# Performance work log

Hardware: AMD Instinct MI355X
Metric: run time of the kernel (lower is better)

The kernel has to match this reference:

```python
import jax, jax.numpy as jnp
import numpy as np

N, E, D, H, C, G = 80000, 1280000, 64, 64, 5, 512


def setup_inputs() -> dict:
    key = jax.random.key(0)
    ks = jax.random.split(key, 8)
    h = jax.random.normal(ks[0], (N, D), jnp.float32)
    src = jax.random.randint(ks[1], (E,), 0, N)
    dst = jax.random.randint(ks[2], (E,), 0, N)
    graph_ids = jnp.sort(jax.random.randint(ks[3], (N,), 0, G))
    # Glorot-ish init for weights
    W1 = jax.random.normal(ks[4], (D, H), jnp.float32) * (1.0 / np.sqrt(D))
    b1 = jnp.zeros((H,), jnp.float32)
    W2 = jax.random.normal(ks[5], (H, H), jnp.float32) * (1.0 / np.sqrt(H))
    b2 = jnp.zeros((H,), jnp.float32)
    Wc = jax.random.normal(ks[6], (H, C), jnp.float32) * (1.0 / np.sqrt(H))
    bc = jnp.zeros((C,), jnp.float32)
    return dict(h=h, src=src, dst=dst, graph_ids=graph_ids,
                W1=W1, b1=b1, W2=W2, b2=b2, Wc=Wc, bc=bc, num_graphs=G)


def reference(h, src, dst, graph_ids, W1, b1, W2, b2, Wc, bc, num_graphs):
    n = h.shape[0]
    ones_e = jnp.ones(src.shape[0], h.dtype)
    # DGL GraphConv norm='both': symmetric normalization, degrees clamped to >=1
    out_deg = jnp.clip(jax.ops.segment_sum(ones_e, src, num_segments=n), 1.0)
    in_deg = jnp.clip(jax.ops.segment_sum(ones_e, dst, num_segments=n), 1.0)
    norm_src = jax.lax.rsqrt(out_deg)  # [N]
    norm_dst = jax.lax.rsqrt(in_deg)   # [N]

    def graph_conv(x, W, b):
        x = x * norm_src[:, None]                                   # scale by D_out^{-1/2}
        agg = jax.ops.segment_sum(x[src], dst, num_segments=n)      # sparse A^T x (copy_u + sum)
        agg = agg * norm_dst[:, None]                               # scale by D_in^{-1/2}
        return agg @ W + b

    h1 = jax.nn.relu(graph_conv(h, W1, b1))
    h2 = jax.nn.relu(graph_conv(h1, W2, b2))

    # dgl.mean_nodes: per-graph mean pooling over nodes
    cnt = jnp.clip(jax.ops.segment_sum(jnp.ones(n, h.dtype), graph_ids,
                                       num_segments=num_graphs), 1.0)
    hg = jax.ops.segment_sum(h2, graph_ids, num_segments=num_graphs) / cnt[:, None]
    return hg @ Wc + bc  # [G, C] logits
```

## Files before the change

### kernel.cpp

```cpp
#include <hip/hip_runtime.h>
#include <hip/hip_bf16.h>


#define NBK 160

typedef __attribute__((ext_vector_type(8))) short bf16x8;
typedef __attribute__((ext_vector_type(4))) float f32x4;

__device__ __forceinline__ float bflo(unsigned u) { return __uint_as_float(u << 16); }
__device__ __forceinline__ float bfhi(unsigned u) { return __uint_as_float(u & 0xffff0000u); }
__device__ __forceinline__ float bf1(unsigned short u) { return __uint_as_float((unsigned)u << 16); }
__device__ __forceinline__ unsigned short f2bf(float f) {
    unsigned u = __float_as_uint(f);
    return (unsigned short)((u + 0x7fff + ((u >> 16) & 1)) >> 16);
}
__device__ __forceinline__ unsigned packbf(float lo, float hi) {
    return (unsigned)f2bf(lo) | ((unsigned)f2bf(hi) << 16);
}

__global__ __launch_bounds__(256) void p1_hist(
    const int* __restrict__ src, const int* __restrict__ dst,
    int* __restrict__ histD, int* __restrict__ histS, int E, int NB)
{
    __shared__ int hd[NBK], hs[NBK];
    for (int i = threadIdx.x; i < NB; i += 256) { hd[i] = 0; hs[i] = 0; }
    __syncthreads();
    int chunk = (E + gridDim.x - 1) / gridDim.x;
    int s0 = blockIdx.x * chunk, s1 = min(E, s0 + chunk);
    for (int i = s0 + threadIdx.x; i < s1; i += 256) {
        atomicAdd(&hd[dst[i] >> 9], 1);
        atomicAdd(&hs[src[i] >> 9], 1);
    }
    __syncthreads();
    for (int b = threadIdx.x; b < NB; b += 256) {
        histD[b * 256 + blockIdx.x] = hd[b];
        histS[b * 256 + blockIdx.x] = hs[b];
    }
}

__global__ __launch_bounds__(256) void p2_scanblocks(
    int* __restrict__ histD, int* __restrict__ histS,
    int* __restrict__ btotD, int* __restrict__ btotS, int NB)
{
    int b = blockIdx.x;
    bool dmode = b < NB;
    int* h = dmode ? (histD + b * 256) : (histS + (b - NB) * 256);
    int t = threadIdx.x, lane = t & 63, w = t >> 6;
    int v = h[t];
    int x = v;
    #pragma unroll
    for (int off = 1; off < 64; off <<= 1) {
        int y = __shfl_up(x, off);
        if (lane >= off) x += y;
    }
    __shared__ int wt[4];
    if (lane == 63) wt[w] = x;
    __syncthreads();
    int bw = 0;
    for (int i = 0; i < w; i++) bw += wt[i];
    h[t] = x - v + bw;
    if (t == 255) (dmode ? btotD : btotS)[dmode ? b : b - NB] = x + bw;
}

__global__ __launch_bounds__(256) void p3_scanbuckets(
    const int* __restrict__ btotD, const int* __restrict__ btotS,
    int* __restrict__ baseD, int* __restrict__ baseS,
    int* __restrict__ row_offs, int E, int NB, int N)
{
    __shared__ int wt[4];
    int t = threadIdx.x, lane = t & 63, w = t >> 6;
    int v = (t < NB) ? btotD[t] : 0;
    int x = v;
    #pragma unroll
    for (int off = 1; off < 64; off <<= 1) {
        int y = __shfl_up(x, off);
        if (lane >= off) x += y;
    }
    if (lane == 63) wt[w] = x;
    __syncthreads();
    int bw = 0;
    for (int i = 0; i < w; i++) bw += wt[i];
    if (t <= NB) baseD[t] = x - v + bw;
    __syncthreads();
    v = (t < NB) ? btotS[t] : 0;
    x = v;
    #pragma unroll
    for (int off = 1; off < 64; off <<= 1) {
        int y = __shfl_up(x, off);
        if (lane >= off) x += y;
    }
    if (lane == 63) wt[w] = x;
    __syncthreads();
    bw = 0;
    for (int i = 0; i < w; i++) bw += wt[i];
    if (t <= NB) baseS[t] = x - v + bw;
    if (t == 0) row_offs[N] = E;
}

__global__ __launch_bounds__(256) void p4_scatter(
    const int* __restrict__ src, const int* __restrict__ dst,
    const int* __restrict__ histD, const int* __restrict__ histS,
    const int* __restrict__ baseD, const int* __restrict__ baseS,
    int* __restrict__ pack, unsigned short* __restrict__ sloc, int E, int NB)
{
    __shared__ int cd[NBK], cs[NBK];
    for (int b = threadIdx.x; b < NB; b += 256) {
        cd[b] = baseD[b] + histD[b * 256 + blockIdx.x];
        cs[b] = baseS[b] + histS[b * 256 + blockIdx.x];
    }
    __syncthreads();
    int chunk = (E + gridDim.x - 1) / gridDim.x;
    int s0 = blockIdx.x * chunk, s1 = min(E, s0 + chunk);
    for (int i = s0 + threadIdx.x; i < s1; i += 256) {
        int s = src[i], d = dst[i];
        int pd = atomicAdd(&cd[d >> 9], 1);
        pack[pd] = ((d & 511) << 17) | s;
        int ps = atomicAdd(&cs[s >> 9], 1);
        sloc[ps] = (unsigned short)(s & 511);
    }
}

__global__ __launch_bounds__(256) void p5_build(
    const int* __restrict__ pack, const unsigned short* __restrict__ sloc,
    const int* __restrict__ baseD, const int* __restrict__ baseS,
    int* __restrict__ col, int* __restrict__ row_offs,
    float* __restrict__ nsrc, float* __restrict__ ndst, int N, int NB)
{
    __shared__ int hist[512];
    __shared__ int wt[4];
    int t = threadIdx.x;
    bool dmode = blockIdx.x < NB;
    int b = dmode ? blockIdx.x : blockIdx.x - NB;
    int n0 = b << 9, n1 = min(N, n0 + 512);
    hist[t] = 0; hist[t + 256] = 0;
    __syncthreads();
    int e0 = dmode ? baseD[b] : baseS[b];
    int e1 = dmode ? baseD[b + 1] : baseS[b + 1];
    if (!dmode) {
        for (int i = e0 + t; i < e1; i += 256)
            atomicAdd(&hist[sloc[i]], 1);
        __syncthreads();
        for (int n = n0 + t; n < n1; n += 256)
            nsrc[n] = rsqrtf((float)max(hist[n - n0], 1));
        return;
    }
    for (int i = e0 + t; i < e1; i += 256)
        atomicAdd(&hist[pack[i] >> 17], 1);
    __syncthreads();
    int c0 = hist[2 * t], c1 = hist[2 * t + 1];
    int v = c0 + c1;
    int lane = t & 63, w = t >> 6;
    int x = v;
    #pragma unroll
    for (int off = 1; off < 64; off <<= 1) {
        int y = __shfl_up(x, off);
        if (lane >= off) x += y;
    }
    if (lane == 63) wt[w] = x;
    __syncthreads();
    int bw = 0;
    for (int i = 0; i < w; i++) bw += wt[i];
    int excl = x - v + bw;
    int n = n0 + 2 * t;
    if (n < n1) {
        row_offs[n] = e0 + excl;
        ndst[n] = rsqrtf((float)max(c0, 1));
    }
    if (n + 1 < n1) {
        row_offs[n + 1] = e0 + excl + c0;
        ndst[n + 1] = rsqrtf((float)max(c1, 1));
    }
    hist[2 * t] = excl;
    hist[2 * t + 1] = excl + c0;
    __syncthreads();
    for (int i = e0 + t; i < e1; i += 256) {
        int wd = pack[i];
        int pos = atomicAdd(&hist[wd >> 17], 1);
        col[e0 + pos] = wd & 0x1FFFF;
    }
}

__global__ __launch_bounds__(256) void bounds_kernel(
    const int* __restrict__ gids, int* __restrict__ goffs, int N, int G)
{
    int i = blockIdx.x * 256 + threadIdx.x;
    if (i >= N) return;
    int b = gids[i];
    if (i == 0) {
        for (int g = 0; g <= b; g++) goffs[g] = 0;
    } else {
        int a = gids[i - 1];
        for (int g = a + 1; g <= b; g++) goffs[g] = i;
    }
    if (i == N - 1) {
        for (int g = b + 1; g <= G; g++) goffs[g] = N;
    }
}

__global__ __launch_bounds__(256) void prescale_kernel(
    const float* __restrict__ h, const float* __restrict__ nsrc,
    unsigned short* __restrict__ xs, int n2)
{
    int i = blockIdx.x * 256 + threadIdx.x;
    if (i >= n2) return;
    float s = nsrc[i >> 5];
    float2 v = ((const float2*)h)[i];
    ushort2 o;
    o.x = f2bf(v.x * s);
    o.y = f2bf(v.y * s);
    ((ushort2*)xs)[i] = o;
}

__global__ __launch_bounds__(256) void gemm_kernel(
    const unsigned short* __restrict__ A, const float* __restrict__ W,
    unsigned short* __restrict__ Z, int M)
{
    int t = threadIdx.x, lane = t & 63, w = t >> 6;
    int col = lane & 15, quad = lane >> 4;
    bf16x8 bfrag[4][2];
    #pragma unroll
    for (int nt = 0; nt < 4; nt++)
        #pragma unroll
        for (int ks = 0; ks < 2; ks++)
            #pragma unroll
            for (int j = 0; j < 8; j++)
                bfrag[nt][ks][j] =
                    (short)f2bf(W[(ks * 32 + quad * 8 + j) * 64 + nt * 16 + col]);

    int mbase = blockIdx.x * 64 + w * 16;
    if (mbase >= M) return;
    int row = min(mbase + col, M - 1);
    const uint4* a4 = (const uint4*)A;
    union { uint4 u; bf16x8 v; } a0, a1;
    a0.u = a4[(size_t)row * 8 + quad];
    a1.u = a4[(size_t)row * 8 + 4 + quad];

    #pragma unroll
    for (int nt = 0; nt < 4; nt++) {
        f32x4 acc = {0.f, 0.f, 0.f, 0.f};
        acc = __builtin_amdgcn_mfma_f32_16x16x32_bf16(a0.v, bfrag[nt][0], acc, 0, 0, 0);
        acc = __builtin_amdgcn_mfma_f32_16x16x32_bf16(a1.v, bfrag[nt][1], acc, 0, 0, 0);
        #pragma unroll
        for (int r = 0; r < 4; r++) {
            int m = mbase + quad * 4 + r;
            if (m < M) Z[(size_t)m * 64 + nt * 16 + col] = f2bf(acc[r]);
        }
    }
}

__global__ __launch_bounds__(256) void agg_kernel(
    const unsigned short* __restrict__ z,
    unsigned short* __restrict__ y,
    const int* __restrict__ col, const int* __restrict__ row_offs,
    const float* __restrict__ nsrc, const float* __restrict__ ndst,
    const float* __restrict__ b, int N, int scale_out)
{
    int lane = threadIdx.x & 63;
    int sub  = lane >> 3;
    int li   = lane & 7;
    float4 bA = ((const float4*)b)[li * 2];
    float4 bB = ((const float4*)b)[li * 2 + 1];
    const uint4* x4 = (const uint4*)z;

    int wid = (blockIdx.x * 256 + threadIdx.x) >> 6;
    int nw  = (gridDim.x * 256) >> 6;
    for (int node = wid; node < N; node += nw) {
        int ro0 = row_offs[node];
        int cnt = row_offs[node + 1] - ro0;
        float a0=0.f,a1=0.f,a2=0.f,a3=0.f,a4=0.f,a5=0.f,a6=0.f,a7=0.f;
        for (int c0 = 0; c0 < cnt; c0 += 64) {
            int m = min(cnt - c0, 64);
            int idx = 0;
            if (lane < m) idx = col[ro0 + c0 + lane];
            for (int i = 0; i < m; i += 16) {
                int e1 = i + sub, e2 = i + 8 + sub;
                int s1 = __shfl(idx, min(e1, m - 1));
                int s2 = __shfl(idx, min(e2, m - 1));
                uint4 v1 = make_uint4(0u,0u,0u,0u), v2 = make_uint4(0u,0u,0u,0u);
                if (e1 < m) v1 = x4[(size_t)s1 * 8 + li];
                if (e2 < m) v2 = x4[(size_t)s2 * 8 + li];
                a0 += bflo(v1.x); a1 += bfhi(v1.x);
                a2 += bflo(v1.y); a3 += bfhi(v1.y);
                a4 += bflo(v1.z); a5 += bfhi(v1.z);
                a6 += bflo(v1.w); a7 += bfhi(v1.w);
                a0 += bflo(v2.x); a1 += bfhi(v2.x);
                a2 += bflo(v2.y); a3 += bfhi(v2.y);
                a4 += bflo(v2.z); a5 += bfhi(v2.z);
                a6 += bflo(v2.w); a7 += bfhi(v2.w);
            }
        }
        #pragma unroll
        for (int off = 8; off <= 32; off <<= 1) {
            a0 += __shfl_xor(a0, off); a1 += __shfl_xor(a1, off);
            a2 += __shfl_xor(a2, off); a3 += __shfl_xor(a3, off);
            a4 += __shfl_xor(a4, off); a5 += __shfl_xor(a5, off);
            a6 += __shfl_xor(a6, off); a7 += __shfl_xor(a7, off);
        }
        float nd = ndst[node];
        float o0 = fmaxf(nd * a0 + bA.x, 0.f);
        float o1 = fmaxf(nd * a1 + bA.y, 0.f);
        float o2 = fmaxf(nd * a2 + bA.z, 0.f);
        float o3 = fmaxf(nd * a3 + bA.w, 0.f);
        float o4 = fmaxf(nd * a4 + bB.x, 0.f);
        float o5 = fmaxf(nd * a5 + bB.y, 0.f);
        float o6 = fmaxf(nd * a6 + bB.z, 0.f);
        float o7 = fmaxf(nd * a7 + bB.w, 0.f);
        if (scale_out) {
            float s = nsrc[node];
            o0 *= s; o1 *= s; o2 *= s; o3 *= s;
            o4 *= s; o5 *= s; o6 *= s; o7 *= s;
        }
        if (sub == 0) {
            uint4 o;
            o.x = packbf(o0, o1);
            o.y = packbf(o2, o3);
            o.z = packbf(o4, o5);
            o.w = packbf(o6, o7);
            ((uint4*)y)[(size_t)node * 8 + li] = o;
        }
    }
}

__global__ __launch_bounds__(256) void pool_kernel(
    const unsigned short* __restrict__ h2, const int* __restrict__ goffs,
    const float* __restrict__ Wc, const float* __restrict__ bc,
    float* __restrict__ out)
{
    int g = blockIdx.x;
    int lane = threadIdx.x & 63;
    int w = threadIdx.x >> 6;
    int s = goffs[g], e = goffs[g + 1];
    float acc = 0.f;
    for (int i = s + w; i < e; i += 4) acc += bf1(h2[i * 64 + lane]);
    __shared__ float red[4][64];
    red[w][lane] = acc;
    __syncthreads();
    if (w == 0) {
        float tot = red[0][lane] + red[1][lane] + red[2][lane] + red[3][lane];
        float mean = tot / (float)max(e - s, 1);
        float wc[5];
        #pragma unroll
        for (int c = 0; c < 5; c++) wc[c] = Wc[lane * 5 + c];
        #pragma unroll
        for (int c = 0; c < 5; c++) {
            float p = mean * wc[c];
            #pragma unroll
            for (int off = 32; off; off >>= 1) p += __shfl_down(p, off);
            if (lane == 0) out[g * 5 + c] = p + bc[c];
        }
    }
}

extern "C" void kernel_launch(void* const* d_in, const int* in_sizes, int n_in,
                              void* d_out, int out_size, void* d_ws, size_t ws_size,
                              hipStream_t stream)
{
    const float* h    = (const float*)d_in[0];
    const int*   src  = (const int*)d_in[1];
    const int*   dst  = (const int*)d_in[2];
    const int*   gids = (const int*)d_in[3];
    const float* W1   = (const float*)d_in[4];
    const float* b1   = (const float*)d_in[5];
    const float* W2   = (const float*)d_in[6];
    const float* b2   = (const float*)d_in[7];
    const float* Wc   = (const float*)d_in[8];
    const float* bc   = (const float*)d_in[9];
    float* out = (float*)d_out;

    const int N = in_sizes[0] / 64;
    const int E = in_sizes[1];
    const int G = out_size / 5;
    const int NB = (N + 511) >> 9;

    auto align = [](size_t x) { return (x + 255) & ~(size_t)255; };
    char* p = (char*)d_ws;
    int* histD   = (int*)p;            p += align((size_t)NBK * 256 * 4);
    int* histS   = (int*)p;            p += align((size_t)NBK * 256 * 4);
    int* btotD   = (int*)p;            p += align((size_t)NBK * 4);
    int* btotS   = (int*)p;            p += align((size_t)NBK * 4);
    int* baseD   = (int*)p;            p += align((size_t)(NBK + 1) * 4);
    int* baseS   = (int*)p;            p += align((size_t)(NBK + 1) * 4);
    int* row_offs= (int*)p;            p += align((size_t)(N + 1) * 4);
    float* nsrc  = (float*)p;          p += align((size_t)N * 4);
    float* ndst  = (float*)p;          p += align((size_t)N * 4);
    int* goffs   = (int*)p;            p += align((size_t)(G + 1) * 4);
    int* pack    = (int*)p;            p += align((size_t)E * 4);
    unsigned short* sloc = (unsigned short*)p; p += align((size_t)E * 2);
    int* col     = (int*)p;            p += align((size_t)E * 4);
    unsigned short* xs  = (unsigned short*)p; p += align((size_t)N * 64 * 2);
    unsigned short* z1  = (unsigned short*)p; p += align((size_t)N * 64 * 2);
    unsigned short* h1s = (unsigned short*)p; p += align((size_t)N * 64 * 2);
    unsigned short* z2  = xs;
    unsigned short* h2  = z1;

    p1_hist<<<256, 256, 0, stream>>>(src, dst, histD, histS, E, NB);
    p2_scanblocks<<<2 * NB, 256, 0, stream>>>(histD, histS, btotD, btotS, NB);
    p3_scanbuckets<<<1, 256, 0, stream>>>(btotD, btotS, baseD, baseS,
                                          row_offs, E, NB, N);
    p4_scatter<<<256, 256, 0, stream>>>(src, dst, histD, histS, baseD, baseS,
                                        pack, sloc, E, NB);
    p5_build<<<2 * NB, 256, 0, stream>>>(pack, sloc, baseD, baseS, col,
                                         row_offs, nsrc, ndst, N, NB);
    bounds_kernel<<<(N + 255) / 256, 256, 0, stream>>>(gids, goffs, N, G);
    prescale_kernel<<<(N * 32 + 255) / 256, 256, 0, stream>>>(h, nsrc, xs, N * 32);

    gemm_kernel<<<(N + 63) / 64, 256, 0, stream>>>(xs, W1, z1, N);
    agg_kernel<<<2048, 256, 0, stream>>>(z1, h1s, col, row_offs,
                                         nsrc, ndst, b1, N, 1);
    gemm_kernel<<<(N + 63) / 64, 256, 0, stream>>>(h1s, W2, z2, N);
    agg_kernel<<<2048, 256, 0, stream>>>(z2, h2, col, row_offs,
                                         nsrc, ndst, b2, N, 0);

    pool_kernel<<<G, 256, 0, stream>>>(h2, goffs, Wc, bc, out);
}
```

Measured before the change: 238.6 us.

## Reorder layers to aggregate before GEMM and fuse prescale/bounds into CSR build

```diff
diff --git a/kernel.cpp b/kernel.cpp
--- a/kernel.cpp
+++ b/kernel.cpp
@@ -3,6 +3,7 @@
 
 
 #define NBK 160
+#define HB  256
 
 typedef __attribute__((ext_vector_type(8))) short bf16x8;
 typedef __attribute__((ext_vector_type(4))) float f32x4;
@@ -20,12 +21,29 @@
 
 __global__ __launch_bounds__(256) void p1_hist(
     const int* __restrict__ src, const int* __restrict__ dst,
-    int* __restrict__ histD, int* __restrict__ histS, int E, int NB)
-{
+    int* __restrict__ histD, int* __restrict__ histS,
+    const int* __restrict__ gids, int* __restrict__ goffs,
+    int E, int NB, int N, int G)
+{
+    if (blockIdx.x >= HB) {
+        int i = (blockIdx.x - HB) * 256 + threadIdx.x;
+        if (i >= N) return;
+        int b = gids[i];
+        if (i == 0) {
+            for (int g = 0; g <= b; g++) goffs[g] = 0;
+        } else {
+            int a = gids[i - 1];
+            for (int g = a + 1; g <= b; g++) goffs[g] = i;
+        }
+        if (i == N - 1) {
+            for (int g = b + 1; g <= G; g++) goffs[g] = N;
+        }
+        return;
+    }
     __shared__ int hd[NBK], hs[NBK];
     for (int i = threadIdx.x; i < NB; i += 256) { hd[i] = 0; hs[i] = 0; }
     __syncthreads();
-    int chunk = (E + gridDim.x - 1) / gridDim.x;
+    int chunk = (E + HB - 1) / HB;
     int s0 = blockIdx.x * chunk, s1 = min(E, s0 + chunk);
     for (int i = s0 + threadIdx.x; i < s1; i += 256) {
         atomicAdd(&hd[dst[i] >> 9], 1);
@@ -124,9 +142,12 @@
     const int* __restrict__ pack, const unsigned short* __restrict__ sloc,
     const int* __restrict__ baseD, const int* __restrict__ baseS,
     int* __restrict__ col, int* __restrict__ row_offs,
-    float* __restrict__ nsrc, float* __restrict__ ndst, int N, int NB)
+    float* __restrict__ nsrc, float* __restrict__ ndst,
+    const float* __restrict__ h, unsigned short* __restrict__ xs,
+    int N, int NB)
 {
     __shared__ int hist[512];
+    __shared__ float nsl[512];
     __shared__ int wt[4];
     int t = threadIdx.x;
     bool dmode = blockIdx.x < NB;
@@ -140,8 +161,24 @@
         for (int i = e0 + t; i < e1; i += 256)
             atomicAdd(&hist[sloc[i]], 1);
         __syncthreads();
-        for (int n = n0 + t; n < n1; n += 256)
-            nsrc[n] = rsqrtf((float)max(hist[n - n0], 1));
+        for (int n = n0 + t; n < n1; n += 256) {
+            float s = rsqrtf((float)max(hist[n - n0], 1));
+            nsrc[n] = s;
+            nsl[n - n0] = s;
+        }
+        __syncthreads();
+        int cnt = n1 - n0;
+        const float2* h2p = (const float2*)h;
+        ushort2* xp = (ushort2*)xs;
+        for (int i = t; i < cnt * 32; i += 256) {
+            int node = i >> 5;
+            float s = nsl[node];
+            float2 v = h2p[(size_t)(n0 + node) * 32 + (i & 31)];
+            ushort2 o;
+            o.x = f2bf(v.x * s);
+            o.y = f2bf(v.y * s);
+            xp[(size_t)(n0 + node) * 32 + (i & 31)] = o;
+        }
         return;
     }
     for (int i = e0 + t; i < e1; i += 256)
@@ -180,86 +217,13 @@
     }
 }
 
-__global__ __launch_bounds__(256) void bounds_kernel(
-    const int* __restrict__ gids, int* __restrict__ goffs, int N, int G)
-{
-    int i = blockIdx.x * 256 + threadIdx.x;
-    if (i >= N) return;
-    int b = gids[i];
-    if (i == 0) {
-        for (int g = 0; g <= b; g++) goffs[g] = 0;
-    } else {
-        int a = gids[i - 1];
-        for (int g = a + 1; g <= b; g++) goffs[g] = i;
-    }
-    if (i == N - 1) {
-        for (int g = b + 1; g <= G; g++) goffs[g] = N;
-    }
-}
-
-__global__ __launch_bounds__(256) void prescale_kernel(
-    const float* __restrict__ h, const float* __restrict__ nsrc,
-    unsigned short* __restrict__ xs, int n2)
-{
-    int i = blockIdx.x * 256 + threadIdx.x;
-    if (i >= n2) return;
-    float s = nsrc[i >> 5];
-    float2 v = ((const float2*)h)[i];
-    ushort2 o;
-    o.x = f2bf(v.x * s);
-    o.y = f2bf(v.y * s);
-    ((ushort2*)xs)[i] = o;
-}
-
-__global__ __launch_bounds__(256) void gemm_kernel(
-    const unsigned short* __restrict__ A, const float* __restrict__ W,
-    unsigned short* __restrict__ Z, int M)
-{
-    int t = threadIdx.x, lane = t & 63, w = t >> 6;
-    int col = lane & 15, quad = lane >> 4;
-    bf16x8 bfrag[4][2];
-    #pragma unroll
-    for (int nt = 0; nt < 4; nt++)
-        #pragma unroll
-        for (int ks = 0; ks < 2; ks++)
-            #pragma unroll
-            for (int j = 0; j < 8; j++)
-                bfrag[nt][ks][j] =
-                    (short)f2bf(W[(ks * 32 + quad * 8 + j) * 64 + nt * 16 + col]);
-
-    int mbase = blockIdx.x * 64 + w * 16;
-    if (mbase >= M) return;
-    int row = min(mbase + col, M - 1);
-    const uint4* a4 = (const uint4*)A;
-    union { uint4 u; bf16x8 v; } a0, a1;
-    a0.u = a4[(size_t)row * 8 + quad];
-    a1.u = a4[(size_t)row * 8 + 4 + quad];
-
-    #pragma unroll
-    for (int nt = 0; nt < 4; nt++) {
-        f32x4 acc = {0.f, 0.f, 0.f, 0.f};
-        acc = __builtin_amdgcn_mfma_f32_16x16x32_bf16(a0.v, bfrag[nt][0], acc, 0, 0, 0);
-        acc = __builtin_amdgcn_mfma_f32_16x16x32_bf16(a1.v, bfrag[nt][1], acc, 0, 0, 0);
-        #pragma unroll
-        for (int r = 0; r < 4; r++) {
-            int m = mbase + quad * 4 + r;
-            if (m < M) Z[(size_t)m * 64 + nt * 16 + col] = f2bf(acc[r]);
-        }
-    }
-}
-
 __global__ __launch_bounds__(256) void agg_kernel(
-    const unsigned short* __restrict__ z,
-    unsigned short* __restrict__ y,
-    const int* __restrict__ col, const int* __restrict__ row_offs,
-    const float* __restrict__ nsrc, const float* __restrict__ ndst,
-    const float* __restrict__ b, int N, int scale_out)
+    const unsigned short* __restrict__ z, unsigned short* __restrict__ y,
+    const int* __restrict__ col, const int* __restrict__ row_offs, int N)
 {
     int lane = threadIdx.x & 63;
     int sub  = lane >> 3;
     int li   = lane & 7;
-    float4 bA = ((const float4*)b)[li * 2];
-    float4 bB = ((const float4*)b)[li * 2 + 1];
     const uint4* x4 = (const uint4*)z;
 
     int wid = (blockIdx.x * 256 + threadIdx.x) >> 6;
@@ -272,13 +236,18 @@
             int m = min(cnt - c0, 64);
             int idx = 0;
             if (lane < m) idx = col[ro0 + c0 + lane];
-            for (int i = 0; i < m; i += 16) {
-                int e1 = i + sub, e2 = i + 8 + sub;
+            for (int i = 0; i < m; i += 32) {
+                int e1 = i + sub, e2 = i + 8 + sub, e3 = i + 16 + sub, e4 = i + 24 + sub;
                 int s1 = __shfl(idx, min(e1, m - 1));
                 int s2 = __shfl(idx, min(e2, m - 1));
+                int s3 = __shfl(idx, min(e3, m - 1));
+                int s4 = __shfl(idx, min(e4, m - 1));
                 uint4 v1 = make_uint4(0u,0u,0u,0u), v2 = make_uint4(0u,0u,0u,0u);
+                uint4 v3 = make_uint4(0u,0u,0u,0u), v4 = make_uint4(0u,0u,0u,0u);
                 if (e1 < m) v1 = x4[(size_t)s1 * 8 + li];
                 if (e2 < m) v2 = x4[(size_t)s2 * 8 + li];
+                if (e3 < m) v3 = x4[(size_t)s3 * 8 + li];
+                if (e4 < m) v4 = x4[(size_t)s4 * 8 + li];
                 a0 += bflo(v1.x); a1 += bfhi(v1.x);
                 a2 += bflo(v1.y); a3 += bfhi(v1.y);
                 a4 += bflo(v1.z); a5 += bfhi(v1.z);
@@ -287,6 +256,14 @@
                 a2 += bflo(v2.y); a3 += bfhi(v2.y);
                 a4 += bflo(v2.z); a5 += bfhi(v2.z);
                 a6 += bflo(v2.w); a7 += bfhi(v2.w);
+                a0 += bflo(v3.x); a1 += bfhi(v3.x);
+                a2 += bflo(v3.y); a3 += bfhi(v3.y);
+                a4 += bflo(v3.z); a5 += bfhi(v3.z);
+                a6 += bflo(v3.w); a7 += bfhi(v3.w);
+                a0 += bflo(v4.x); a1 += bfhi(v4.x);
+                a2 += bflo(v4.y); a3 += bfhi(v4.y);
+                a4 += bflo(v4.z); a5 += bfhi(v4.z);
+                a6 += bflo(v4.w); a7 += bfhi(v4.w);
             }
         }
         #pragma unroll
@@ -296,27 +273,65 @@
             a4 += __shfl_xor(a4, off); a5 += __shfl_xor(a5, off);
             a6 += __shfl_xor(a6, off); a7 += __shfl_xor(a7, off);
         }
-        float nd = ndst[node];
-        float o0 = fmaxf(nd * a0 + bA.x, 0.f);
-        float o1 = fmaxf(nd * a1 + bA.y, 0.f);
-        float o2 = fmaxf(nd * a2 + bA.z, 0.f);
-        float o3 = fmaxf(nd * a3 + bA.w, 0.f);
-        float o4 = fmaxf(nd * a4 + bB.x, 0.f);
-        float o5 = fmaxf(nd * a5 + bB.y, 0.f);
-        float o6 = fmaxf(nd * a6 + bB.z, 0.f);
-        float o7 = fmaxf(nd * a7 + bB.w, 0.f);
-        if (scale_out) {
-            float s = nsrc[node];
-            o0 *= s; o1 *= s; o2 *= s; o3 *= s;
-            o4 *= s; o5 *= s; o6 *= s; o7 *= s;
-        }
         if (sub == 0) {
             uint4 o;
-            o.x = packbf(o0, o1);
-            o.y = packbf(o2, o3);
-            o.z = packbf(o4, o5);
-            o.w = packbf(o6, o7);
+            o.x = packbf(a0, a1);
+            o.y = packbf(a2, a3);
+            o.z = packbf(a4, a5);
+            o.w = packbf(a6, a7);
             ((uint4*)y)[(size_t)node * 8 + li] = o;
+        }
+    }
+}
+
+__global__ __launch_bounds__(256) void gemm_kernel(
+    const unsigned short* __restrict__ A, const float* __restrict__ W,
+    const float* __restrict__ b, const float* __restrict__ ndst,
+    const float* __restrict__ nsrc, unsigned short* __restrict__ Z,
+    int M, int scale_out)
+{
+    int t = threadIdx.x, lane = t & 63, w = t >> 6;
+    int col = lane & 15, quad = lane >> 4;
+    bf16x8 bfrag[4][2];
+    #pragma unroll
+    for (int nt = 0; nt < 4; nt++)
+        #pragma unroll
+        for (int ks = 0; ks < 2; ks++)
+            #pragma unroll
+            for (int j = 0; j < 8; j++)
+                bfrag[nt][ks][j] =
+                    (short)f2bf(W[(ks * 32 + quad * 8 + j) * 64 + nt * 16 + col]);
+    float bias[4];
+    #pragma unroll
+    for (int nt = 0; nt < 4; nt++) bias[nt] = b[nt * 16 + col];
+
+    int mbase = blockIdx.x * 64 + w * 16;
+    if (mbase >= M) return;
+    int row = min(mbase + col, M - 1);
+    const uint4* a4 = (const uint4*)A;
+    union { uint4 u; bf16x8 v; } a0, a1;
+    a0.u = a4[(size_t)row * 8 + quad];
+    a1.u = a4[(size_t)row * 8 + 4 + quad];
+
+    float nd[4], ns[4];
+    #pragma unroll
+    for (int r = 0; r < 4; r++) {
+        int m = min(mbase + quad * 4 + r, M - 1);
+        nd[r] = ndst[m];
+        ns[r] = scale_out ? nsrc[m] : 1.f;
+    }
+
+    #pragma unroll
+    for (int nt = 0; nt < 4; nt++) {
+        f32x4 acc = {0.f, 0.f, 0.f, 0.f};
+        acc = __builtin_amdgcn_mfma_f32_16x16x32_bf16(a0.v, bfrag[nt][0], acc, 0, 0, 0);
+        acc = __builtin_amdgcn_mfma_f32_16x16x32_bf16(a1.v, bfrag[nt][1], acc, 0, 0, 0);
+        #pragma unroll
+        for (int r = 0; r < 4; r++) {
+            int m = mbase + quad * 4 + r;
+            if (m < M)
+                Z[(size_t)m * 64 + nt * 16 + col] =
+                    f2bf(fmaxf(nd[r] * acc[r] + bias[nt], 0.f) * ns[r]);
         }
     }
 }
@@ -371,6 +386,7 @@
     const int E = in_sizes[1];
     const int G = out_size / 5;
     const int NB = (N + 511) >> 9;
+    const int NBB = (N + 255) / 256;
 
     auto align = [](size_t x) { return (x + 255) & ~(size_t)255; };
     char* p = (char*)d_ws;
@@ -388,28 +404,27 @@
     unsigned short* sloc = (unsigned short*)p; p += align((size_t)E * 2);
     int* col     = (int*)p;            p += align((size_t)E * 4);
     unsigned short* xs  = (unsigned short*)p; p += align((size_t)N * 64 * 2);
-    unsigned short* z1  = (unsigned short*)p; p += align((size_t)N * 64 * 2);
+    unsigned short* s1  = (unsigned short*)p; p += align((size_t)N * 64 * 2);
     unsigned short* h1s = (unsigned short*)p; p += align((size_t)N * 64 * 2);
-    unsigned short* z2  = xs;
-    unsigned short* h2  = z1;
-
-    p1_hist<<<256, 256, 0, stream>>>(src, dst, histD, histS, E, NB);
+    unsigned short* s2  = s1;
+    unsigned short* h2  = xs;
+
+    p1_hist<<<HB + NBB, 256, 0, stream>>>(src, dst, histD, histS,
+                                          gids, goffs, E, NB, N, G);
     p2_scanblocks<<<2 * NB, 256, 0, stream>>>(histD, histS, btotD, btotS, NB);
     p3_scanbuckets<<<1, 256, 0, stream>>>(btotD, btotS, baseD, baseS,
                                           row_offs, E, NB, N);
     p4_scatter<<<256, 256, 0, stream>>>(src, dst, histD, histS, baseD, baseS,
                                         pack, sloc, E, NB);
     p5_build<<<2 * NB, 256, 0, stream>>>(pack, sloc, baseD, baseS, col,
-                                         row_offs, nsrc, ndst, N, NB);
-    bounds_kernel<<<(N + 255) / 256, 256, 0, stream>>>(gids, goffs, N, G);
-    prescale_kernel<<<(N * 32 + 255) / 256, 256, 0, stream>>>(h, nsrc, xs, N * 32);
-
-    gemm_kernel<<<(N + 63) / 64, 256, 0, stream>>>(xs, W1, z1, N);
-    agg_kernel<<<2048, 256, 0, stream>>>(z1, h1s, col, row_offs,
-                                         nsrc, ndst, b1, N, 1);
-    gemm_kernel<<<(N + 63) / 64, 256, 0, stream>>>(h1s, W2, z2, N);
-    agg_kernel<<<2048, 256, 0, stream>>>(z2, h2, col, row_offs,
-                                         nsrc, ndst, b2, N, 0);
+                                         row_offs, nsrc, ndst, h, xs, N, NB);
+
+    agg_kernel<<<2048, 256, 0, stream>>>(xs, s1, col, row_offs, N);
+    gemm_kernel<<<(N + 63) / 64, 256, 0, stream>>>(s1, W1, b1, ndst, nsrc,
+                                                   h1s, N, 1);
+    agg_kernel<<<2048, 256, 0, stream>>>(h1s, s2, col, row_offs, N);
+    gemm_kernel<<<(N + 63) / 64, 256, 0, stream>>>(s2, W2, b2, ndst, nsrc,
+                                                   h2, N, 0);
 
     pool_kernel<<<G, 256, 0, stream>>>(h2, goffs, Wc, bc, out);
 }
```

Result: no change. 238.4 us (-0.1%).
